# Kernel optimization log

Hardware: AMD Instinct MI355X
Metric: run time of the kernel (lower is better)

## Reference

```python
import jax, jax.numpy as jnp
import numpy as np

B, N, D = 4, 1024, 1024
NH = 16
HS = D // NH
HID = 4 * D
EPS = 1e-5

def layernorm(x, w, b):
    mu = jnp.mean(x, axis=-1, keepdims=True)
    var = jnp.mean(jnp.square(x - mu), axis=-1, keepdims=True)
    return (x - mu) * jax.lax.rsqrt(var + EPS) * w + b

def setup_inputs() -> dict:
    key = jax.random.key(0)
    ks = jax.random.split(key, 8)
    s = lambda fan_in: 1.0 / np.sqrt(fan_in)
    return {
        "x": jax.random.normal(ks[0], (B, N, D), jnp.float32),
        "qkv_w": jax.random.uniform(ks[1], (3 * D, D), jnp.float32, -s(D), s(D)),
        "proj_w": jax.random.uniform(ks[2], (D, D), jnp.float32, -s(D), s(D)),
        "proj_b": jax.random.uniform(ks[3], (D,), jnp.float32, -s(D), s(D)),
        "ln1_w": jnp.ones((D,), jnp.float32),
        "ln1_b": jnp.zeros((D,), jnp.float32),
        "fc1_w": jax.random.uniform(ks[4], (HID, D), jnp.float32, -s(D), s(D)),
        "fc1_b": jax.random.uniform(ks[5], (HID,), jnp.float32, -s(D), s(D)),
        "fc2_w": jax.random.uniform(ks[6], (D, HID), jnp.float32, -s(HID), s(HID)),
        "fc2_b": jax.random.uniform(ks[7], (D,), jnp.float32, -s(HID), s(HID)),
        "ln2_w": jnp.ones((D,), jnp.float32),
        "ln2_b": jnp.zeros((D,), jnp.float32),
    }

def attention(x, qkv_w, proj_w, proj_b):
    # x: [b, n, d]; qkv linear (no bias), split into q,k,v per head
    qkv = jnp.einsum('bnd,ed->bne', x, qkv_w)              # [b, n, 3d]
    qkv = qkv.reshape(B, N, 3, NH, HS).transpose(2, 0, 3, 1, 4)  # [3, b, nh, n, hs]
    q, k, v = qkv[0], qkv[1], qkv[2]
    scale = HS ** -0.5
    # mask=False => self.mask == 1, so (mask-1)*LARGE_NUMBER == 0
    att = jax.nn.softmax(scale * jnp.einsum('bhqe,bhke->bhqk', q, k), axis=-1)
    y = jnp.einsum('bhqk,bhke->bhqe', att, v)              # [b, nh, n, hs]
    y = y.transpose(0, 2, 1, 3).reshape(B, N, D)
    return jnp.einsum('bnd,ed->bne', y, proj_w) + proj_b

def mlp(x, fc1_w, fc1_b, fc2_w, fc2_b):
    h = jax.nn.gelu(jnp.einsum('bnd,hd->bnh', x, fc1_w) + fc1_b, approximate=False)
    return jnp.einsum('bnh,dh->bnd', h, fc2_w) + fc2_b

def reference(x, qkv_w, proj_w, proj_b, ln1_w, ln1_b, fc1_w, fc1_b, fc2_w, fc2_b, ln2_w, ln2_b):
    x = x + attention(layernorm(x, ln1_w, ln1_b), qkv_w, proj_w, proj_b)
    x = x + mlp(layernorm(x, ln2_w, ln2_b), fc1_w, fc1_b, fc2_w, fc2_b)
    return x
```

## Files before the change

kernel.cpp:

```cpp
#include <hip/hip_runtime.h>
#include <hip/hip_bf16.h>

typedef __attribute__((ext_vector_type(8))) short short8;
typedef __attribute__((ext_vector_type(8))) unsigned short ushort8;
typedef __attribute__((ext_vector_type(4))) float floatx4;

#define DEV static __device__ __forceinline__

DEV unsigned short f2bf(float f) {
  unsigned int u = __builtin_bit_cast(unsigned int, f);
  u += 0x7fff + ((u >> 16) & 1);
  return (unsigned short)(u >> 16);
}
DEV float bf2f(unsigned short u) {
  return __builtin_bit_cast(float, (unsigned int)u << 16);
}

DEV void gload_lds16(const void* g, void* l) {
  __builtin_amdgcn_global_load_lds(
      (const __attribute__((address_space(1))) unsigned int*)g,
      (__attribute__((address_space(3))) unsigned int*)l, 16, 0, 0);
}

__global__ __launch_bounds__(256) void cvt4_kernel(const float* __restrict__ w0,
                                                   const float* __restrict__ w1,
                                                   const float* __restrict__ w2,
                                                   const float* __restrict__ w3,
                                                   unsigned short* __restrict__ o0,
                                                   unsigned short* __restrict__ o1,
                                                   unsigned short* __restrict__ o2,
                                                   unsigned short* __restrict__ o3) {
  int i = blockIdx.x * 256 + threadIdx.x;
  const float* in; unsigned short* out; int j;
  if (i < 786432)       { in = w0; out = o0; j = i; }
  else if (i < 1048576) { in = w1; out = o1; j = i - 786432; }
  else if (i < 2097152) { in = w2; out = o2; j = i - 1048576; }
  else                  { in = w3; out = o3; j = i - 2097152; }
  float4 v = reinterpret_cast<const float4*>(in)[j];
  ushort4 o;
  o.x = f2bf(v.x); o.y = f2bf(v.y); o.z = f2bf(v.z); o.w = f2bf(v.w);
  reinterpret_cast<ushort4*>(out)[j] = o;
}

__global__ __launch_bounds__(256) void ln_kernel(const float* __restrict__ x,
                                                 const float* __restrict__ w,
                                                 const float* __restrict__ b,
                                                 unsigned short* __restrict__ out) {
  const int row = blockIdx.x;
  const float* xr = x + (size_t)row * 1024;
  float4 v = reinterpret_cast<const float4*>(xr)[threadIdx.x];
  float s  = v.x + v.y + v.z + v.w;
  float ss = v.x*v.x + v.y*v.y + v.z*v.z + v.w*v.w;
  #pragma unroll
  for (int off = 1; off < 64; off <<= 1) {
    s  += __shfl_xor(s, off);
    ss += __shfl_xor(ss, off);
  }
  __shared__ float red[8];
  const int wid = threadIdx.x >> 6, lane = threadIdx.x & 63;
  if (lane == 0) { red[wid] = s; red[4 + wid] = ss; }
  __syncthreads();
  s  = red[0] + red[1] + red[2] + red[3];
  ss = red[4] + red[5] + red[6] + red[7];
  const float mu  = s * (1.0f / 1024.0f);
  const float var = ss * (1.0f / 1024.0f) - mu * mu;
  const float rstd = rsqrtf(var + 1e-5f);
  float4 wv = reinterpret_cast<const float4*>(w)[threadIdx.x];
  float4 bv = reinterpret_cast<const float4*>(b)[threadIdx.x];
  ushort4 o;
  o.x = f2bf((v.x - mu) * rstd * wv.x + bv.x);
  o.y = f2bf((v.y - mu) * rstd * wv.y + bv.y);
  o.z = f2bf((v.z - mu) * rstd * wv.z + bv.z);
  o.w = f2bf((v.w - mu) * rstd * wv.w + bv.w);
  reinterpret_cast<ushort4*>(out)[(size_t)row * 256 + threadIdx.x] = o;
}

template<int EPI>
__global__ __launch_bounds__(512, 2) void gemm256(const unsigned short* __restrict__ A,
                                                  const unsigned short* __restrict__ Bw,
                                                  unsigned short* __restrict__ outb,
                                                  const float* __restrict__ bias,
                                                  int K, int N, int NT) {
  __shared__ unsigned short As[2][256 * 64];
  __shared__ unsigned short Bs[2][256 * 64];
  const int tid = threadIdx.x, lane = tid & 63, wid = tid >> 6;
  const int wr = wid >> 2, wc = wid & 3;
  const int fr = lane & 15, s0 = lane >> 4;

  const int nwg = gridDim.x;
  const int qq = nwg >> 3, rr8 = nwg & 7, xcd = blockIdx.x & 7, lid = blockIdx.x >> 3;
  const int wg = (xcd < rr8 ? xcd * (qq + 1) : rr8 * (qq + 1) + (xcd - rr8) * qq) + lid;
  const int brow = (wg / NT) * 256, bcol = (wg % NT) * 256;

  const unsigned short* ag[4];
  const unsigned short* bg[4];
  #pragma unroll
  for (int L = 0; L < 4; L++) {
    const int idx = L * 512 + tid;
    const int row = idx >> 3;
    const int ss  = ((idx & 7) ^ (row & 7)) * 8;
    ag[L] = A  + (size_t)(brow + row) * K + ss;
    bg[L] = Bw + (size_t)(bcol + row) * K + ss;
  }
  const int ldst = tid * 8;

  #define STG256(kt, buf)                                                     \
    do {                                                                      \
      const int ko = (kt) * 64;                                               \
      gload_lds16(ag[0] + ko, &As[buf][ldst]);                                \
      gload_lds16(ag[1] + ko, &As[buf][4096 + ldst]);                         \
      gload_lds16(ag[2] + ko, &As[buf][8192 + ldst]);                         \
      gload_lds16(ag[3] + ko, &As[buf][12288 + ldst]);                        \
      gload_lds16(bg[0] + ko, &Bs[buf][ldst]);                                \
      gload_lds16(bg[1] + ko, &Bs[buf][4096 + ldst]);                         \
      gload_lds16(bg[2] + ko, &Bs[buf][8192 + ldst]);                         \
      gload_lds16(bg[3] + ko, &Bs[buf][12288 + ldst]);                        \
    } while (0)

  const int xs = fr & 7;
  const int aoff = (wr * 128 + fr) * 64;
  const int boff = (wc * 64 + fr) * 64;
  const int sl0 = ((0 + s0) ^ xs) * 8;
  const int sl1 = ((4 + s0) ^ xs) * 8;

  floatx4 acc[8][4];
  #pragma unroll
  for (int m = 0; m < 8; m++)
    #pragma unroll
    for (int n = 0; n < 4; n++) acc[m][n] = (floatx4){0.f, 0.f, 0.f, 0.f};

  const int NTK = K >> 6;
  STG256(0, 0);

  for (int kt = 0; kt < NTK; ++kt) {
    const int cur = kt & 1;
    if (kt + 1 < NTK) {
      STG256(kt + 1, cur ^ 1);
      asm volatile("s_waitcnt vmcnt(8)" ::: "memory");
    } else {
      asm volatile("s_waitcnt vmcnt(0)" ::: "memory");
    }
    __builtin_amdgcn_s_barrier();

    const unsigned short* Ac = As[cur];
    const unsigned short* Bc = Bs[cur];
    short8 a0[4][2], a1[4][2], b0[2][2], b1[2][2];

    #pragma unroll
    for (int m = 0; m < 4; m++) {
      a0[m][0] = *reinterpret_cast<const short8*>(Ac + aoff + m * 1024 + sl0);
      a0[m][1] = *reinterpret_cast<const short8*>(Ac + aoff + m * 1024 + sl1);
    }
    #pragma unroll
    for (int n = 0; n < 2; n++) {
      b0[n][0] = *reinterpret_cast<const short8*>(Bc + boff + n * 1024 + sl0);
      b0[n][1] = *reinterpret_cast<const short8*>(Bc + boff + n * 1024 + sl1);
    }
    __builtin_amdgcn_s_barrier();
    __builtin_amdgcn_s_setprio(1);
    #pragma unroll
    for (int m = 0; m < 4; m++)
      #pragma unroll
      for (int n = 0; n < 2; n++) {
        acc[m][n] = __builtin_amdgcn_mfma_f32_16x16x32_bf16(a0[m][0], b0[n][0], acc[m][n], 0, 0, 0);
        acc[m][n] = __builtin_amdgcn_mfma_f32_16x16x32_bf16(a0[m][1], b0[n][1], acc[m][n], 0, 0, 0);
      }
    __builtin_amdgcn_s_setprio(0);
    __builtin_amdgcn_s_barrier();

    #pragma unroll
    for (int n = 0; n < 2; n++) {
      b1[n][0] = *reinterpret_cast<const short8*>(Bc + boff + (n + 2) * 1024 + sl0);
      b1[n][1] = *reinterpret_cast<const short8*>(Bc + boff + (n + 2) * 1024 + sl1);
    }
    __builtin_amdgcn_s_barrier();
    __builtin_amdgcn_s_setprio(1);
    #pragma unroll
    for (int m = 0; m < 4; m++)
      #pragma unroll
      for (int n = 0; n < 2; n++) {
        acc[m][n + 2] = __builtin_amdgcn_mfma_f32_16x16x32_bf16(a0[m][0], b1[n][0], acc[m][n + 2], 0, 0, 0);
        acc[m][n + 2] = __builtin_amdgcn_mfma_f32_16x16x32_bf16(a0[m][1], b1[n][1], acc[m][n + 2], 0, 0, 0);
      }
    __builtin_amdgcn_s_setprio(0);
    __builtin_amdgcn_s_barrier();

    #pragma unroll
    for (int m = 0; m < 4; m++) {
      a1[m][0] = *reinterpret_cast<const short8*>(Ac + aoff + (m + 4) * 1024 + sl0);
      a1[m][1] = *reinterpret_cast<const short8*>(Ac + aoff + (m + 4) * 1024 + sl1);
    }
    __builtin_amdgcn_s_barrier();
    __builtin_amdgcn_s_setprio(1);
    #pragma unroll
    for (int m = 0; m < 4; m++)
      #pragma unroll
      for (int n = 0; n < 2; n++) {
        acc[m + 4][n] = __builtin_amdgcn_mfma_f32_16x16x32_bf16(a1[m][0], b0[n][0], acc[m + 4][n], 0, 0, 0);
        acc[m + 4][n] = __builtin_amdgcn_mfma_f32_16x16x32_bf16(a1[m][1], b0[n][1], acc[m + 4][n], 0, 0, 0);
      }
    __builtin_amdgcn_s_setprio(0);
    __builtin_amdgcn_s_barrier();

    __builtin_amdgcn_s_setprio(1);
    #pragma unroll
    for (int m = 0; m < 4; m++)
      #pragma unroll
      for (int n = 0; n < 2; n++) {
        acc[m + 4][n + 2] = __builtin_amdgcn_mfma_f32_16x16x32_bf16(a1[m][0], b1[n][0], acc[m + 4][n + 2], 0, 0, 0);
        acc[m + 4][n + 2] = __builtin_amdgcn_mfma_f32_16x16x32_bf16(a1[m][1], b1[n][1], acc[m + 4][n + 2], 0, 0, 0);
      }
    __builtin_amdgcn_s_setprio(0);
    __builtin_amdgcn_s_barrier();
  }
  #undef STG256

  #pragma unroll
  for (int m = 0; m < 8; m++) {
    #pragma unroll
    for (int n = 0; n < 4; n++) {
      const int col = bcol + wc * 64 + n * 16 + fr;
      #pragma unroll
      for (int r = 0; r < 4; r++) {
        const size_t idx = (size_t)(brow + wr * 128 + m * 16 + s0 * 4 + r) * N + col;
        float v = acc[m][n][r];
        if (EPI == 1) {
          v += bias[col];
          const float u = v * 0.7978845608f * (1.0f + 0.044715f * v * v);
          const float e = __expf(2.0f * u);
          v = v * (e / (e + 1.0f));
        }
        outb[idx] = f2bf(v);
      }
    }
  }
}

__global__ __launch_bounds__(512) void gemm128sk(const unsigned short* __restrict__ A,
                                                 const unsigned short* __restrict__ Bw,
                                                 unsigned short* __restrict__ outb,
                                                 int K, int Ksl, int N, int NT, int ntiles) {
  __shared__ unsigned short As[4][128 * 32];
  __shared__ unsigned short Bs[4][128 * 32];
  const int tid = threadIdx.x, lane = tid & 63, wid = tid >> 6;
  const int wrow = (wid >> 2) * 64, wcol = (wid & 3) * 32;
  const int fr = lane & 15, s0 = lane >> 4;

  const int nwg = gridDim.x;
  const int qq = nwg >> 3, rr8 = nwg & 7, xcd = blockIdx.x & 7, lid = blockIdx.x >> 3;
  const int wg = (xcd < rr8 ? xcd * (qq + 1) : rr8 * (qq + 1) + (xcd - rr8) * qq) + lid;
  const int kslice = wg / ntiles, t = wg % ntiles;
  const int brow = (t / NT) * 128, bcol = (t % NT) * 128;
  const int kofs = kslice * Ksl;

  const int srow = tid >> 2;
  const int sslot = ((tid & 3) ^ ((srow >> 1) & 3)) * 8;
  const unsigned short* ag = A  + (size_t)(brow + srow) * K + kofs + sslot;
  const unsigned short* bg = Bw + (size_t)(bcol + srow) * K + kofs + sslot;
  const int ldst = tid * 8;

  #define STG(kt, buf)                              \
    do {                                            \
      const int ko = (kt) * 32;                     \
      gload_lds16(ag + ko, &As[buf][ldst]);         \
      gload_lds16(bg + ko, &Bs[buf][ldst]);         \
    } while (0)

  const int slr = (s0 ^ ((fr >> 1) & 3)) * 8;

  floatx4 acc[4][2];
  #pragma unroll
  for (int i = 0; i < 4; i++)
    #pragma unroll
    for (int j = 0; j < 2; j++) acc[i][j] = (floatx4){0.f, 0.f, 0.f, 0.f};

  const int NTK = Ksl >> 5;
  STG(0, 0);
  STG(1, 1);
  STG(2, 2);

  for (int kt = 0; kt < NTK; ++kt) {
    const int cur = kt & 3;
    if (kt + 3 < NTK) {
      STG(kt + 3, (kt + 3) & 3);
      asm volatile("s_waitcnt vmcnt(6)" ::: "memory");
    } else if (kt + 2 < NTK) {
      asm volatile("s_waitcnt vmcnt(4)" ::: "memory");
    } else if (kt + 1 < NTK) {
      asm volatile("s_waitcnt vmcnt(2)" ::: "memory");
    } else {
      asm volatile("s_waitcnt vmcnt(0)" ::: "memory");
    }
    __builtin_amdgcn_s_barrier();

    short8 af[4], bf[2];
    #pragma unroll
    for (int i = 0; i < 4; i++)
      af[i] = *reinterpret_cast<const short8*>(&As[cur][(wrow + i * 16 + fr) * 32 + slr]);
    #pragma unroll
    for (int j = 0; j < 2; j++)
      bf[j] = *reinterpret_cast<const short8*>(&Bs[cur][(wcol + j * 16 + fr) * 32 + slr]);
    __builtin_amdgcn_s_setprio(1);
    #pragma unroll
    for (int i = 0; i < 4; i++)
      #pragma unroll
      for (int j = 0; j < 2; j++)
        acc[i][j] = __builtin_amdgcn_mfma_f32_16x16x32_bf16(af[i], bf[j], acc[i][j], 0, 0, 0);
    __builtin_amdgcn_s_setprio(0);
    __builtin_amdgcn_s_barrier();
  }
  #undef STG

  unsigned short* po = outb + (size_t)kslice * ((size_t)ntiles * 16384);
  const int erow = brow + wrow + (s0 << 2);
  const int ecol = bcol + wcol + fr;
  #pragma unroll
  for (int i = 0; i < 4; i++)
    #pragma unroll
    for (int j = 0; j < 2; j++)
      #pragma unroll
      for (int r = 0; r < 4; r++)
        po[(size_t)(erow + i * 16 + r) * N + ecol + j * 16] = f2bf(acc[i][j][r]);
}

__global__ __launch_bounds__(256) void red_ln(const unsigned short* __restrict__ p0,
                                              const unsigned short* __restrict__ p1,
                                              const float* __restrict__ x,
                                              const float* __restrict__ bias,
                                              const float* __restrict__ lw,
                                              const float* __restrict__ lb,
                                              float* __restrict__ x1,
                                              unsigned short* __restrict__ xn) {
  const int row = blockIdx.x, t = threadIdx.x;
  const size_t o4 = (size_t)row * 256 + t;
  ushort4 a = reinterpret_cast<const ushort4*>(p0)[o4];
  ushort4 c = reinterpret_cast<const ushort4*>(p1)[o4];
  float4 xv = reinterpret_cast<const float4*>(x)[o4];
  float4 bv = reinterpret_cast<const float4*>(bias)[t];
  float4 v;
  v.x = bf2f(a.x) + bf2f(c.x) + bv.x + xv.x;
  v.y = bf2f(a.y) + bf2f(c.y) + bv.y + xv.y;
  v.z = bf2f(a.z) + bf2f(c.z) + bv.z + xv.z;
  v.w = bf2f(a.w) + bf2f(c.w) + bv.w + xv.w;
  reinterpret_cast<float4*>(x1)[o4] = v;

  float s  = v.x + v.y + v.z + v.w;
  float ss = v.x*v.x + v.y*v.y + v.z*v.z + v.w*v.w;
  #pragma unroll
  for (int off = 1; off < 64; off <<= 1) {
    s  += __shfl_xor(s, off);
    ss += __shfl_xor(ss, off);
  }
  __shared__ float red[8];
  const int wid = t >> 6, lane = t & 63;
  if (lane == 0) { red[wid] = s; red[4 + wid] = ss; }
  __syncthreads();
  s  = red[0] + red[1] + red[2] + red[3];
  ss = red[4] + red[5] + red[6] + red[7];
  const float mu  = s * (1.0f / 1024.0f);
  const float var = ss * (1.0f / 1024.0f) - mu * mu;
  const float rstd = rsqrtf(var + 1e-5f);
  float4 wv = reinterpret_cast<const float4*>(lw)[t];
  float4 lv = reinterpret_cast<const float4*>(lb)[t];
  ushort4 o;
  o.x = f2bf((v.x - mu) * rstd * wv.x + lv.x);
  o.y = f2bf((v.y - mu) * rstd * wv.y + lv.y);
  o.z = f2bf((v.z - mu) * rstd * wv.z + lv.z);
  o.w = f2bf((v.w - mu) * rstd * wv.w + lv.w);
  reinterpret_cast<ushort4*>(xn)[o4] = o;
}

__global__ __launch_bounds__(256) void red_out(const unsigned short* __restrict__ p0,
                                               const unsigned short* __restrict__ p1,
                                               const float* __restrict__ x1,
                                               const float* __restrict__ bias,
                                               float* __restrict__ out) {
  const size_t i4 = (size_t)blockIdx.x * 256 + threadIdx.x;
  const int c4 = (int)(i4 & 255);
  ushort4 a = reinterpret_cast<const ushort4*>(p0)[i4];
  ushort4 c = reinterpret_cast<const ushort4*>(p1)[i4];
  float4 xv = reinterpret_cast<const float4*>(x1)[i4];
  float4 bv = reinterpret_cast<const float4*>(bias)[c4];
  float4 v;
  v.x = bf2f(a.x) + bf2f(c.x) + bv.x + xv.x;
  v.y = bf2f(a.y) + bf2f(c.y) + bv.y + xv.y;
  v.z = bf2f(a.z) + bf2f(c.z) + bv.z + xv.z;
  v.w = bf2f(a.w) + bf2f(c.w) + bv.w + xv.w;
  reinterpret_cast<float4*>(out)[i4] = v;
}

__global__ __launch_bounds__(256) void vtrans_kernel(const unsigned short* __restrict__ qkv,
                                                     unsigned short* __restrict__ vt) {
  __shared__ unsigned short T[64][66];
  const int nt = blockIdx.x, bh = blockIdx.y;
  const int b = bh >> 4, h = bh & 15;
  const unsigned short* src = qkv + (size_t)b * 1024 * 3072 + 2048 + h * 64;
  const int r = threadIdx.x >> 3, s = threadIdx.x & 7;
  ushort8 a0 = *reinterpret_cast<const ushort8*>(src + (size_t)(nt * 64 + r) * 3072 + s * 8);
  ushort8 a1 = *reinterpret_cast<const ushort8*>(src + (size_t)(nt * 64 + r + 32) * 3072 + s * 8);
  #pragma unroll
  for (int j = 0; j < 8; j++) {
    T[r][s * 8 + j]      = a0[j];
    T[r + 32][s * 8 + j] = a1[j];
  }
  __syncthreads();
  ushort8 o0, o1;
  #pragma unroll
  for (int j = 0; j < 8; j++) {
    o0[j] = T[s * 8 + j][r];
    o1[j] = T[s * 8 + j][r + 32];
  }
  unsigned short* dst = vt + (size_t)bh * 64 * 1024 + nt * 64 + s * 8;
  *reinterpret_cast<ushort8*>(dst + (size_t)r * 1024)        = o0;
  *reinterpret_cast<ushort8*>(dst + (size_t)(r + 32) * 1024) = o1;
}

__global__ __launch_bounds__(512) void attn_kernel(const unsigned short* __restrict__ qkv,
                                                   const unsigned short* __restrict__ vt,
                                                   unsigned short* __restrict__ y) {
  __shared__ unsigned short Ks[2][64 * 64];
  __shared__ unsigned short Vs[2][64 * 64];
  __shared__ unsigned short Ps[8][16 * 64];

  const int tid = threadIdx.x;
  const int lane = tid & 63;
  const int w = tid >> 6;
  const int wg = (blockIdx.x & 7) * 64 + (blockIdx.x >> 3);
  const int bh = wg >> 3, qt = wg & 7;
  const int b = bh >> 4, h = bh & 15;
  const int fr = lane & 15, s0 = lane >> 4;
  const int sw = fr & 7;
  const size_t RS = 3072;

  const unsigned short* qbase = qkv + (size_t)b * 1024 * RS + h * 64;
  const unsigned short* kbase = qbase + 1024;
  const unsigned short* vbase = vt + (size_t)bh * 64 * 1024;

  short8 aq[2];
  {
    const unsigned short* qrow = qbase + (size_t)(qt * 128 + w * 16 + fr) * RS;
    aq[0] = *reinterpret_cast<const short8*>(qrow + s0 * 8);
    aq[1] = *reinterpret_cast<const short8*>(qrow + 32 + s0 * 8);
  }

  const float SC = 0.125f * 1.44269504089f;
  float m_run[4], l_run[4];
  floatx4 accy[4];
  #pragma unroll
  for (int r = 0; r < 4; r++) { m_run[r] = -1e30f; l_run[r] = 0.f; }
  #pragma unroll
  for (int d = 0; d < 4; d++) accy[d] = (floatx4){0.f, 0.f, 0.f, 0.f};

  const int krow = tid >> 3, kslot = tid & 7;
  const int gslot = (kslot ^ (krow & 7)) * 8;
  const unsigned short* kg = kbase + (size_t)krow * RS + gslot;
  const unsigned short* vg = vbase + (size_t)krow * 1024 + gslot;

  #define STAGE(t, buf)                                       \
    do {                                                      \
      gload_lds16(kg + (size_t)(t) * 64 * RS, &Ks[buf][tid * 8]); \
      gload_lds16(vg + (size_t)(t) * 64,      &Vs[buf][tid * 8]); \
    } while (0)

  STAGE(0, 0);
  int cur = 0;

  for (int kt = 0; kt < 16; ++kt) {
    if (kt < 15) {
      STAGE(kt + 1, cur ^ 1);
      asm volatile("s_waitcnt vmcnt(2)" ::: "memory");
    } else {
      asm volatile("s_waitcnt vmcnt(0)" ::: "memory");
    }
    __builtin_amdgcn_s_barrier();

    const unsigned short* Kt = Ks[cur];
    const unsigned short* Vc = Vs[cur];

    floatx4 sfr[4];
    __builtin_amdgcn_s_setprio(1);
    #pragma unroll
    for (int f = 0; f < 4; ++f) {
      const unsigned short* krw = Kt + (f * 16 + fr) * 64;
      short8 kb0 = *reinterpret_cast<const short8*>(krw + (((s0)     ^ sw) << 3));
      short8 kb1 = *reinterpret_cast<const short8*>(krw + (((s0 + 4) ^ sw) << 3));
      floatx4 s = (floatx4){0.f, 0.f, 0.f, 0.f};
      s = __builtin_amdgcn_mfma_f32_16x16x32_bf16(aq[0], kb0, s, 0, 0, 0);
      s = __builtin_amdgcn_mfma_f32_16x16x32_bf16(aq[1], kb1, s, 0, 0, 0);
      sfr[f] = s * SC;
    }
    __builtin_amdgcn_s_setprio(0);

    float mv[4];
    #pragma unroll
    for (int r = 0; r < 4; r++) {
      float t = fmaxf(fmaxf(sfr[0][r], sfr[1][r]), fmaxf(sfr[2][r], sfr[3][r]));
      #pragma unroll
      for (int m = 1; m < 16; m <<= 1) t = fmaxf(t, __shfl_xor(t, m));
      mv[r] = t;
    }
    bool grow = (mv[0] > m_run[0] + 8.f) || (mv[1] > m_run[1] + 8.f) ||
                (mv[2] > m_run[2] + 8.f) || (mv[3] > m_run[3] + 8.f);
    if (__any(grow)) {
      #pragma unroll
      for (int r = 0; r < 4; r++) {
        const float mn = fmaxf(m_run[r], mv[r]);
        const float alpha = exp2f(m_run[r] - mn);
        m_run[r] = mn;
        l_run[r] *= alpha;
        #pragma unroll
        for (int d = 0; d < 4; d++) accy[d][r] *= alpha;
      }
    }

    #pragma unroll
    for (int r = 0; r < 4; r++) {
      const int q = s0 * 4 + r;
      const int qx = (q & 7) << 3;
      float ps = 0.f;
      #pragma unroll
      for (int f = 0; f < 4; f++) {
        float p = exp2f(sfr[f][r] - m_run[r]);
        ps += p;
        Ps[w][q * 64 + ((f * 16 + fr) ^ qx)] = f2bf(p);
      }
      #pragma unroll
      for (int m = 1; m < 16; m <<= 1) ps += __shfl_xor(ps, m);
      l_run[r] += ps;
    }

    __builtin_amdgcn_s_setprio(1);
    #pragma unroll
    for (int ks = 0; ks < 2; ++ks) {
      const int sA = ((ks * 4 + s0) ^ sw) << 3;
      short8 ap = *reinterpret_cast<const short8*>(&Ps[w][fr * 64 + sA]);
      #pragma unroll
      for (int j = 0; j < 4; ++j) {
        short8 vb = *reinterpret_cast<const short8*>(Vc + (j * 16 + fr) * 64 + sA);
        accy[j] = __builtin_amdgcn_mfma_f32_16x16x32_bf16(ap, vb, accy[j], 0, 0, 0);
      }
    }
    __builtin_amdgcn_s_setprio(0);
    __builtin_amdgcn_s_barrier();
    cur ^= 1;
  }
  #undef STAGE

  #pragma unroll
  for (int r = 0; r < 4; r++) {
    const float inv = 1.0f / l_run[r];
    const size_t grow2 =
        (size_t)(b * 1024 + qt * 128 + w * 16 + s0 * 4 + r) * 1024 + h * 64;
    #pragma unroll
    for (int d = 0; d < 4; ++d)
      y[grow2 + d * 16 + fr] = f2bf(accy[d][r] * inv);
  }
}

extern "C" void kernel_launch(void* const* d_in, const int* in_sizes, int n_in,
                              void* d_out, int out_size, void* d_ws, size_t ws_size,
                              hipStream_t stream) {
  const float* x      = (const float*)d_in[0];
  const float* qkv_w  = (const float*)d_in[1];
  const float* proj_w = (const float*)d_in[2];
  const float* proj_b = (const float*)d_in[3];
  const float* ln1_w  = (const float*)d_in[4];
  const float* ln1_b  = (const float*)d_in[5];
  const float* fc1_w  = (const float*)d_in[6];
  const float* fc1_b  = (const float*)d_in[7];
  const float* fc2_w  = (const float*)d_in[8];
  const float* fc2_b  = (const float*)d_in[9];
  const float* ln2_w  = (const float*)d_in[10];
  const float* ln2_b  = (const float*)d_in[11];
  float* out = (float*)d_out;

  char* ws = (char*)d_ws;
  unsigned short* qkvw16  = (unsigned short*)(ws + 0);
  unsigned short* projw16 = (unsigned short*)(ws + 6291456);
  unsigned short* fc1w16  = (unsigned short*)(ws + 8388608);
  unsigned short* fc2w16  = (unsigned short*)(ws + 16777216);
  float*          x1      = (float*)(ws + 25165824);
  unsigned short* vt      = (unsigned short*)(ws + 25165824);
  unsigned short* xn      = (unsigned short*)(ws + 41943040);
  unsigned short* big     = (unsigned short*)(ws + 50331648);
  unsigned short* pp      = big;
  unsigned short* fp      = (unsigned short*)(ws + 0);

  cvt4_kernel<<<12288, 256, 0, stream>>>(qkv_w, proj_w, fc1_w, fc2_w,
                                         qkvw16, projw16, fc1w16, fc2w16);

  ln_kernel<<<4096, 256, 0, stream>>>(x, ln1_w, ln1_b, xn);
  gemm256<0><<<192, 512, 0, stream>>>(xn, qkvw16, big, nullptr, 1024, 3072, 12);
  vtrans_kernel<<<dim3(16, 64), 256, 0, stream>>>(big, vt);
  attn_kernel<<<512, 512, 0, stream>>>(big, vt, xn);
  gemm128sk<<<512, 512, 0, stream>>>(xn, projw16, pp, 1024, 512, 1024, 8, 256);
  red_ln<<<4096, 256, 0, stream>>>(pp, pp + 4194304, x, proj_b, ln2_w, ln2_b, x1, xn);
  gemm256<1><<<256, 512, 0, stream>>>(xn, fc1w16, big, fc1_b, 1024, 4096, 16);
  gemm128sk<<<512, 512, 0, stream>>>(big, fc2w16, fp, 4096, 2048, 1024, 8, 256);
  red_out<<<4096, 256, 0, stream>>>(fp, fp + 4194304, x1, fc2_b, out);
}
```

Before: 249.7 us.

## Transpose QK^T MFMA so each lane owns one query row in attention

Swaps the MFMA operand order so the score tile is transposed and each lane holds a single query's scores. Row max and sum then need only two cross-lane shuffles instead of four-step reductions per row. The softmax scale is folded into Q once at load time, and probabilities are packed with v_cvt_pk_bf16 and stored as 64-bit words in a re-swizzled LDS layout. The trade-off is extra shuffles to broadcast alpha and the final 1/l back to the accumulator layout, plus an extra bf16 rounding of scaled Q.

```diff
diff --git a/kernel.cpp b/kernel.cpp
--- a/kernel.cpp
+++ b/kernel.cpp
@@ -14,6 +14,11 @@
 }
 DEV float bf2f(unsigned short u) {
   return __builtin_bit_cast(float, (unsigned int)u << 16);
+}
+DEV unsigned int cvtpk_bf16(float lo, float hi) {
+  unsigned int r;
+  asm("v_cvt_pk_bf16_f32 %0, %1, %2" : "=v"(r) : "v"(lo), "v"(hi));
+  return r;
 }
 
 DEV void gload_lds16(const void* g, void* l) {
@@ -420,7 +425,7 @@
                                                    unsigned short* __restrict__ y) {
   __shared__ unsigned short Ks[2][64 * 64];
   __shared__ unsigned short Vs[2][64 * 64];
-  __shared__ unsigned short Ps[8][16 * 64];
+  __shared__ unsigned long long Pq[8][256];
 
   const int tid = threadIdx.x;
   const int lane = tid & 63;
@@ -436,18 +441,24 @@
   const unsigned short* kbase = qbase + 1024;
   const unsigned short* vbase = vt + (size_t)bh * 64 * 1024;
 
+  const float SC = 0.125f * 1.44269504089f;
+
   short8 aq[2];
   {
     const unsigned short* qrow = qbase + (size_t)(qt * 128 + w * 16 + fr) * RS;
-    aq[0] = *reinterpret_cast<const short8*>(qrow + s0 * 8);
-    aq[1] = *reinterpret_cast<const short8*>(qrow + 32 + s0 * 8);
-  }
-
-  const float SC = 0.125f * 1.44269504089f;
-  float m_run[4], l_run[4];
+    ushort8 q0 = *reinterpret_cast<const ushort8*>(qrow + s0 * 8);
+    ushort8 q1 = *reinterpret_cast<const ushort8*>(qrow + 32 + s0 * 8);
+    #pragma unroll
+    for (int i = 0; i < 8; i++) {
+      q0[i] = f2bf(bf2f(q0[i]) * SC);
+      q1[i] = f2bf(bf2f(q1[i]) * SC);
+    }
+    aq[0] = __builtin_bit_cast(short8, q0);
+    aq[1] = __builtin_bit_cast(short8, q1);
+  }
+
+  float m_run = -1e30f, l_run = 0.f;
   floatx4 accy[4];
-  #pragma unroll
-  for (int r = 0; r < 4; r++) { m_run[r] = -1e30f; l_run[r] = 0.f; }
   #pragma unroll
   for (int d = 0; d < 4; d++) accy[d] = (floatx4){0.f, 0.f, 0.f, 0.f};
 
@@ -456,8 +467,8 @@
   const unsigned short* kg = kbase + (size_t)krow * RS + gslot;
   const unsigned short* vg = vbase + (size_t)krow * 1024 + gslot;
 
-  #define STAGE(t, buf)                                       \
-    do {                                                      \
+  #define STAGE(t, buf)                                           \
+    do {                                                          \
       gload_lds16(kg + (size_t)(t) * 64 * RS, &Ks[buf][tid * 8]); \
       gload_lds16(vg + (size_t)(t) * 64,      &Vs[buf][tid * 8]); \
     } while (0)
@@ -477,7 +488,7 @@
     const unsigned short* Kt = Ks[cur];
     const unsigned short* Vc = Vs[cur];
 
-    floatx4 sfr[4];
+    floatx4 st[4];
     __builtin_amdgcn_s_setprio(1);
     #pragma unroll
     for (int f = 0; f < 4; ++f) {
@@ -485,55 +496,67 @@
       short8 kb0 = *reinterpret_cast<const short8*>(krw + (((s0)     ^ sw) << 3));
       short8 kb1 = *reinterpret_cast<const short8*>(krw + (((s0 + 4) ^ sw) << 3));
       floatx4 s = (floatx4){0.f, 0.f, 0.f, 0.f};
-      s = __builtin_amdgcn_mfma_f32_16x16x32_bf16(aq[0], kb0, s, 0, 0, 0);
-      s = __builtin_amdgcn_mfma_f32_16x16x32_bf16(aq[1], kb1, s, 0, 0, 0);
-      sfr[f] = s * SC;
+      s = __builtin_amdgcn_mfma_f32_16x16x32_bf16(kb0, aq[0], s, 0, 0, 0);
+      s = __builtin_amdgcn_mfma_f32_16x16x32_bf16(kb1, aq[1], s, 0, 0, 0);
+      st[f] = s;
     }
     __builtin_amdgcn_s_setprio(0);
 
-    float mv[4];
-    #pragma unroll
-    for (int r = 0; r < 4; r++) {
-      float t = fmaxf(fmaxf(sfr[0][r], sfr[1][r]), fmaxf(sfr[2][r], sfr[3][r]));
-      #pragma unroll
-      for (int m = 1; m < 16; m <<= 1) t = fmaxf(t, __shfl_xor(t, m));
-      mv[r] = t;
-    }
-    bool grow = (mv[0] > m_run[0] + 8.f) || (mv[1] > m_run[1] + 8.f) ||
-                (mv[2] > m_run[2] + 8.f) || (mv[3] > m_run[3] + 8.f);
-    if (__any(grow)) {
-      #pragma unroll
-      for (int r = 0; r < 4; r++) {
-        const float mn = fmaxf(m_run[r], mv[r]);
-        const float alpha = exp2f(m_run[r] - mn);
-        m_run[r] = mn;
-        l_run[r] *= alpha;
-        #pragma unroll
-        for (int d = 0; d < 4; d++) accy[d][r] *= alpha;
+    float pm;
+    {
+      float m0 = fmaxf(fmaxf(st[0][0], st[0][1]), fmaxf(st[0][2], st[0][3]));
+      float m1 = fmaxf(fmaxf(st[1][0], st[1][1]), fmaxf(st[1][2], st[1][3]));
+      float m2 = fmaxf(fmaxf(st[2][0], st[2][1]), fmaxf(st[2][2], st[2][3]));
+      float m3 = fmaxf(fmaxf(st[3][0], st[3][1]), fmaxf(st[3][2], st[3][3]));
+      pm = fmaxf(fmaxf(m0, m1), fmaxf(m2, m3));
+      pm = fmaxf(pm, __shfl_xor(pm, 16));
+      pm = fmaxf(pm, __shfl_xor(pm, 32));
+    }
+    if (__any(pm > m_run + 8.f)) {
+      const float mn = fmaxf(m_run, pm);
+      const float alpha = exp2f(m_run - mn);
+      m_run = mn;
+      l_run *= alpha;
+      float a0 = __shfl(alpha, s0 * 4 + 0);
+      float a1 = __shfl(alpha, s0 * 4 + 1);
+      float a2 = __shfl(alpha, s0 * 4 + 2);
+      float a3 = __shfl(alpha, s0 * 4 + 3);
+      #pragma unroll
+      for (int j = 0; j < 4; j++) {
+        accy[j][0] *= a0; accy[j][1] *= a1; accy[j][2] *= a2; accy[j][3] *= a3;
       }
     }
 
-    #pragma unroll
-    for (int r = 0; r < 4; r++) {
-      const int q = s0 * 4 + r;
-      const int qx = (q & 7) << 3;
-      float ps = 0.f;
-      #pragma unroll
-      for (int f = 0; f < 4; f++) {
-        float p = exp2f(sfr[f][r] - m_run[r]);
-        ps += p;
-        Ps[w][q * 64 + ((f * 16 + fr) ^ qx)] = f2bf(p);
-      }
-      #pragma unroll
-      for (int m = 1; m < 16; m <<= 1) ps += __shfl_xor(ps, m);
-      l_run[r] += ps;
-    }
+    float ps = 0.f;
+    unsigned long long pk[4];
+    #pragma unroll
+    for (int f = 0; f < 4; f++) {
+      float p0 = exp2f(st[f][0] - m_run);
+      float p1 = exp2f(st[f][1] - m_run);
+      float p2 = exp2f(st[f][2] - m_run);
+      float p3 = exp2f(st[f][3] - m_run);
+      ps += (p0 + p1) + (p2 + p3);
+      unsigned int lo = cvtpk_bf16(p0, p1);
+      unsigned int hi = cvtpk_bf16(p2, p3);
+      pk[f] = (unsigned long long)lo | ((unsigned long long)hi << 32);
+    }
+    ps += __shfl_xor(ps, 16);
+    ps += __shfl_xor(ps, 32);
+    l_run += ps;
+
+    #pragma unroll
+    for (int f = 0; f < 4; f++)
+      Pq[w][(f * 4 + s0) * 16 + (fr ^ (s0 << 2))] = pk[f];
 
     __builtin_amdgcn_s_setprio(1);
     #pragma unroll
     for (int ks = 0; ks < 2; ++ks) {
+      const int b0 = ks * 8 + s0 * 2, b1 = b0 + 1;
+      unsigned long long q0 = Pq[w][b0 * 16 + (fr ^ ((b0 & 3) << 2))];
+      unsigned long long q1 = Pq[w][b1 * 16 + (fr ^ ((b1 & 3) << 2))];
+      ulonglong2 u; u.x = q0; u.y = q1;
+      short8 ap = __builtin_bit_cast(short8, u);
       const int sA = ((ks * 4 + s0) ^ sw) << 3;
-      short8 ap = *reinterpret_cast<const short8*>(&Ps[w][fr * 64 + sA]);
       #pragma unroll
       for (int j = 0; j < 4; ++j) {
         short8 vb = *reinterpret_cast<const short8*>(Vc + (j * 16 + fr) * 64 + sA);
@@ -546,14 +569,16 @@
   }
   #undef STAGE
 
+  float linv[4];
+  #pragma unroll
+  for (int r = 0; r < 4; r++) linv[r] = 1.0f / __shfl(l_run, s0 * 4 + r);
   #pragma unroll
   for (int r = 0; r < 4; r++) {
-    const float inv = 1.0f / l_run[r];
     const size_t grow2 =
         (size_t)(b * 1024 + qt * 128 + w * 16 + s0 * 4 + r) * 1024 + h * 64;
     #pragma unroll
-    for (int d = 0; d < 4; ++d)
-      y[grow2 + d * 16 + fr] = f2bf(accy[d][r] * inv);
+    for (int j = 0; j < 4; ++j)
+      y[grow2 + j * 16 + fr] = f2bf(accy[j][r] * linv[r]);
   }
 }
 
```

After: 232.2 us. 7.0% less time.
